# Performance work log

Measured on AMD Instinct MI355X. Metric: run time of the kernel, lower is better.

The kernel has to match this reference:

```python
import jax, jax.numpy as jnp
import numpy as np

B, T, D, H = 4, 2048, 1024, 16
HD = D // H  # 64

def setup_inputs() -> dict:
    key = jax.random.key(0)
    ks = jax.random.split(key, 6)
    s = 0.02
    x = jax.random.normal(ks[0], (B, T, D), dtype=jnp.float32)
    # per-head projection weights, torch Linear layout [out=HD, in=D], stacked over heads
    Wq = jax.random.normal(ks[1], (H, HD, D), dtype=jnp.float32) * s
    Wk = jax.random.normal(ks[2], (H, HD, D), dtype=jnp.float32) * s
    Wv = jax.random.normal(ks[3], (H, HD, D), dtype=jnp.float32) * s
    Wo = jax.random.normal(ks[4], (D, D), dtype=jnp.float32) * s
    bo = jax.random.normal(ks[5], (D,), dtype=jnp.float32) * s
    return {"x": x, "Wq": Wq, "Wk": Wk, "Wv": Wv, "Wo": Wo, "bo": bo}

def reference(x, Wq, Wk, Wv, Wo, bo):
    # per-head projections (same math as per-head nn.Linear, vectorized over heads)
    Q = jnp.einsum('btd,hkd->bhtk', x, Wq)
    K = jnp.einsum('bsd,hkd->bhsk', x, Wk)
    V = jnp.einsum('bsd,hkd->bhsk', x, Wv)
    scale = 1.0 / jnp.sqrt(jnp.asarray(HD, x.dtype))
    logits = jnp.einsum('bhtk,bhsk->bhts', Q, K) * scale  # [B,H,T,S]
    w = jax.nn.softmax(logits, axis=-1)
    out = jnp.einsum('bhts,bhsk->bhtk', w, V)  # [B,H,T,HD]
    # concat heads in order -> [B,T,D]
    cat = jnp.transpose(out, (0, 2, 1, 3)).reshape(B, T, D)
    return cat @ Wo.T + bo
```

## Files before the change

kernel.cpp:

```cpp
#include <hip/hip_runtime.h>
#include <hip/hip_bf16.h>
#include <stdint.h>
#include <math.h>

typedef unsigned short u16;
typedef uint32_t u32;
typedef __bf16 bf16x8 __attribute__((ext_vector_type(8)));
typedef float f32x4 __attribute__((ext_vector_type(4)));
typedef float f32x16 __attribute__((ext_vector_type(16)));
typedef u16 u16x8 __attribute__((ext_vector_type(8)));
typedef u16 u16x4 __attribute__((ext_vector_type(4)));

#define B_ 4
#define T_ 2048
#define D_ 1024
#define H_ 16
#define HD_ 64
#define M_ (B_*T_)

__device__ __forceinline__ u16 f2bf(float f) {
    union { __bf16 h; u16 u; } c;
    c.h = (__bf16)f;
    return c.u;
}

__device__ __forceinline__ void gl16(const u16* g, u16* l) {
    __builtin_amdgcn_global_load_lds(
        (__attribute__((address_space(1))) void*)g,
        (__attribute__((address_space(3))) void*)l, 16, 0, 0);
}

__device__ __forceinline__ f32x4 mfma16(bf16x8 a, bf16x8 b, f32x4 c) {
    return __builtin_amdgcn_mfma_f32_16x16x32_bf16(a, b, c, 0, 0, 0);
}

__device__ __forceinline__ f32x16 mfma32(bf16x8 a, bf16x8 b, f32x16 c) {
    return __builtin_amdgcn_mfma_f32_32x32x16_bf16(a, b, c, 0, 0, 0);
}

__device__ __forceinline__ u32 cvtpk_bf16(float lo, float hi) {
    u32 r;
    asm("v_cvt_pk_bf16_f32 %0, %1, %2" : "=v"(r) : "v"(lo), "v"(hi));
    return r;
}

__device__ __forceinline__ float fexp2(float x) {
    return __builtin_amdgcn_exp2f(x);
}

__global__ __launch_bounds__(256) void precast(
    const float* __restrict__ x,  const float* __restrict__ wq,
    const float* __restrict__ wk, const float* __restrict__ wv,
    const float* __restrict__ wo,
    u16* __restrict__ xb, u16* __restrict__ wqb, u16* __restrict__ wkb,
    u16* __restrict__ wvb, u16* __restrict__ wob)
{
    const int i = (blockIdx.x * 256 + threadIdx.x) * 4;
    const int nx = M_ * D_;
    const float* src; u16* dst; int off;
    if (i < nx) { src = x; dst = xb; off = i; }
    else {
        int j = i - nx;
        int w = j >> 20;
        off = j & ((1 << 20) - 1);
        switch (w) {
            case 0: src = wq; dst = wqb; break;
            case 1: src = wk; dst = wkb; break;
            case 2: src = wv; dst = wvb; break;
            default: src = wo; dst = wob; break;
        }
    }
    float4 v = *(const float4*)&src[off];
    u16x4 p = { f2bf(v.x), f2bf(v.y), f2bf(v.z), f2bf(v.w) };
    *(u16x4*)&dst[off] = p;
}

__device__ __forceinline__ void gemm8_pipe(
    const u16* __restrict__ Xg, const u16* __restrict__ Wg,
    u16* As, u16* Bs,
    const int tid, const int wm, const int wn, const int l15, const int quad,
    f32x4 acc[4][4])
{
    const u16* asrc[4]; int adst[4];
#pragma unroll
    for (int i = 0; i < 4; ++i) {
        int c = tid + i * 512;
        int row = c >> 3, slot = c & 7;
        asrc[i] = Xg + (size_t)row * 1024 + (slot ^ (row & 7)) * 8;
        adst[i] = c * 8;
    }
    const u16* bsrc[2]; int bdst[2];
#pragma unroll
    for (int i = 0; i < 2; ++i) {
        int c = tid + i * 512;
        int row = c >> 3, slot = c & 7;
        bsrc[i] = Wg + (size_t)row * 1024 + (slot ^ (row & 7)) * 8;
        bdst[i] = c * 8;
    }
    const int sw = l15 & 7;
    const int so0 = (quad ^ sw) * 8;
    const int so1 = ((4 + quad) ^ sw) * 8;

#pragma unroll
    for (int tt = 0; tt < 2; ++tt) {
#pragma unroll
        for (int i = 0; i < 4; ++i) gl16(asrc[i] + tt * 64, As + tt * 16384 + adst[i]);
#pragma unroll
        for (int i = 0; i < 2; ++i) gl16(bsrc[i] + tt * 64, Bs + tt * 8192 + bdst[i]);
    }
    asm volatile("s_waitcnt vmcnt(6)" ::: "memory");
    __builtin_amdgcn_s_barrier();

#pragma unroll
    for (int t = 0; t < 16; ++t) {
        const u16* Ab = As + (t % 3) * 16384;
        const u16* Bb = Bs + (t % 3) * 8192;
        if (t + 2 < 16) {
            const int k2 = (t + 2) * 64;
            u16* An = As + ((t + 2) % 3) * 16384;
            u16* Bn = Bs + ((t + 2) % 3) * 8192;
#pragma unroll
            for (int i = 0; i < 4; ++i) gl16(asrc[i] + k2, An + adst[i]);
#pragma unroll
            for (int i = 0; i < 2; ++i) gl16(bsrc[i] + k2, Bn + bdst[i]);
        }
        __builtin_amdgcn_sched_barrier(0);
        bf16x8 af0[4], af1[4], bf0[4], bf1[4];
#pragma unroll
        for (int mf = 0; mf < 4; ++mf) {
            const int rr = (wm * 64 + mf * 16 + l15) * 64;
            af0[mf] = *(const bf16x8*)&Ab[rr + so0];
            af1[mf] = *(const bf16x8*)&Ab[rr + so1];
        }
#pragma unroll
        for (int nf = 0; nf < 4; ++nf) {
            const int rr = (wn * 64 + nf * 16 + l15) * 64;
            bf0[nf] = *(const bf16x8*)&Bb[rr + so0];
            bf1[nf] = *(const bf16x8*)&Bb[rr + so1];
        }
        __builtin_amdgcn_s_setprio(1);
#pragma unroll
        for (int mf = 0; mf < 4; ++mf)
#pragma unroll
            for (int nf = 0; nf < 4; ++nf)
                acc[mf][nf] = mfma16(af0[mf], bf0[nf], acc[mf][nf]);
#pragma unroll
        for (int mf = 0; mf < 4; ++mf)
#pragma unroll
            for (int nf = 0; nf < 4; ++nf)
                acc[mf][nf] = mfma16(af1[mf], bf1[nf], acc[mf][nf]);
        __builtin_amdgcn_s_setprio(0);
        __builtin_amdgcn_sched_barrier(0);
        if (t + 2 < 16)      asm volatile("s_waitcnt vmcnt(6)" ::: "memory");
        else if (t + 1 < 16) asm volatile("s_waitcnt vmcnt(0)" ::: "memory");
        __builtin_amdgcn_s_barrier();
    }
}

__global__ __launch_bounds__(512, 2) void qkv_gemm(
    const u16* __restrict__ Xb, const u16* __restrict__ W3,
    u16* __restrict__ Qo, u16* __restrict__ Ko, u16* __restrict__ Vt)
{
    __shared__ __attribute__((aligned(16))) u16 As[3 * 256 * 64];
    __shared__ __attribute__((aligned(16))) u16 Bs[3 * 128 * 64];

    const int wg = blockIdx.x + 24 * blockIdx.y;
    const int xcd = wg & 7, k = wg >> 3;
    const int by = xcd * 4 + (k / 24);
    const int bx = k % 24;
    const int n0 = bx * 128, m0 = by * 256;
    const u16* Xg = Xb + (size_t)m0 * 1024;
    const u16* Wg = W3 + (size_t)n0 * 1024;
    const int z = n0 >> 10;
    const float qs = (z == 0) ? 0.125f * 1.44269504088896340736f : 1.0f;

    const int tid = threadIdx.x;
    const int lane = tid & 63;
    const int wave = tid >> 6;
    const int wm = wave >> 1, wn = wave & 1;
    const int l15 = lane & 15, quad = lane >> 4;

    f32x4 acc[4][4];
#pragma unroll
    for (int i = 0; i < 4; ++i)
#pragma unroll
        for (int j = 0; j < 4; ++j) acc[i][j] = (f32x4){0.f, 0.f, 0.f, 0.f};

    gemm8_pipe(Xg, Wg, &As[0], &Bs[0], tid, wm, wn, l15, quad, acc);

    if (z == 2) {
#pragma unroll
        for (int mf = 0; mf < 4; ++mf)
#pragma unroll
            for (int nf = 0; nf < 4; ++nf) {
                int row0 = m0 + wm * 64 + mf * 16 + quad * 4;
                int colz = (n0 & 1023) + wn * 64 + nf * 16 + l15;
                int b = row0 >> 11;
                int t = row0 & 2047;
                int h = colz >> 6;
                int hd = colz & 63;
                u16x4 pv = { f2bf(acc[mf][nf][0]), f2bf(acc[mf][nf][1]),
                             f2bf(acc[mf][nf][2]), f2bf(acc[mf][nf][3]) };
                *(u16x4*)&Vt[(((size_t)(b * H_ + h) * HD_ + hd)) * T_ + t] = pv;
            }
    } else {
        u16* Out = (z == 0) ? Qo : Ko;
#pragma unroll
        for (int mf = 0; mf < 4; ++mf)
#pragma unroll
            for (int nf = 0; nf < 4; ++nf)
#pragma unroll
                for (int r = 0; r < 4; ++r) {
                    int row = m0 + wm * 64 + mf * 16 + quad * 4 + r;
                    int colz = (n0 & 1023) + wn * 64 + nf * 16 + l15;
                    int b = row >> 11;
                    int t = row & 2047;
                    int h = colz >> 6;
                    int hd = colz & 63;
                    Out[((b * H_ + h) * T_ + t) * HD_ + hd] = f2bf(acc[mf][nf][r] * qs);
                }
    }
}

__global__ __launch_bounds__(512, 2) void out_gemm(
    const u16* __restrict__ Xb, const u16* __restrict__ W3,
    const float* __restrict__ bias, float* __restrict__ Out)
{
    __shared__ __attribute__((aligned(16))) u16 As[3 * 256 * 64];
    __shared__ __attribute__((aligned(16))) u16 Bs[3 * 128 * 64];

    const int wg = blockIdx.x + 8 * blockIdx.y;
    const int xcd = wg & 7, k = wg >> 3;
    const int by = xcd * 4 + (k / 8);
    const int bx = k & 7;
    const int n0 = bx * 128, m0 = by * 256;
    const u16* Xg = Xb + (size_t)m0 * 1024;
    const u16* Wg = W3 + (size_t)n0 * 1024;

    const int tid = threadIdx.x;
    const int lane = tid & 63;
    const int wave = tid >> 6;
    const int wm = wave >> 1, wn = wave & 1;
    const int l15 = lane & 15, quad = lane >> 4;

    f32x4 acc[4][4];
#pragma unroll
    for (int i = 0; i < 4; ++i)
#pragma unroll
        for (int j = 0; j < 4; ++j) acc[i][j] = (f32x4){0.f, 0.f, 0.f, 0.f};

    gemm8_pipe(Xg, Wg, &As[0], &Bs[0], tid, wm, wn, l15, quad, acc);

#pragma unroll
    for (int mf = 0; mf < 4; ++mf)
#pragma unroll
        for (int nf = 0; nf < 4; ++nf)
#pragma unroll
            for (int r = 0; r < 4; ++r) {
                int row = m0 + wm * 64 + mf * 16 + quad * 4 + r;
                int col = n0 + wn * 64 + nf * 16 + l15;
                Out[(size_t)row * 1024 + col] = acc[mf][nf][r] + bias[col];
            }
}

__global__ __launch_bounds__(512, 2) void attn(
    const u16* __restrict__ Q, const u16* __restrict__ K,
    const u16* __restrict__ Vt_g, u16* __restrict__ O)
{
    __shared__ __attribute__((aligned(16))) u16 Ks[3 * 4096];
    __shared__ __attribute__((aligned(16))) u16 Vts[3 * 4096];
    __shared__ float lps[8 * 64];

    const int tid = threadIdx.x;
    const int lane = tid & 63, w = tid >> 6;
    const int l31 = lane & 31, hi = lane >> 5;

    const int wg = blockIdx.x + (T_ / 512) * (blockIdx.y + H_ * blockIdx.z);
    const int xcd = wg & 7, k8 = wg >> 3;
    const int bh = xcd + 8 * (k8 >> 2);
    const int xq = k8 & 3;
    const int b = bh >> 4, h = bh & 15;
    const int t0 = xq * 512 + w * 64;

    const size_t base = (size_t)bh * T_ * HD_;
    const u16* Kb = K + base;
    const u16* Vtb = Vt_g + base;
    const u16* Qb = Q + base + (size_t)t0 * HD_;

    const int ra = tid >> 3, sa = (tid & 7) ^ (ra & 7);
    const u16* kp = Kb  + (size_t)ra * 64 + sa * 8;
    const u16* vp = Vtb + (size_t)ra * T_ + sa * 8;
    const int ldst = tid * 8;

    int foff[2][4];
#pragma unroll
    for (int nt = 0; nt < 2; ++nt) {
        const int row = nt * 32 + l31;
#pragma unroll
        for (int kb = 0; kb < 4; ++kb)
            foff[nt][kb] = row * 64 + (((kb * 2 + hi) ^ (row & 7)) * 8);
    }

    bf16x8 qf[2][4];
#pragma unroll
    for (int qt = 0; qt < 2; ++qt)
#pragma unroll
        for (int kb = 0; kb < 4; ++kb)
            qf[qt][kb] = *(const bf16x8*)&Qb[(qt * 32 + l31) * 64 + kb * 16 + hi * 8];

    f32x16 zacc;
#pragma unroll
    for (int i = 0; i < 16; ++i) zacc[i] = 0.f;
    f32x16 oacc[2][2];
#pragma unroll
    for (int qt = 0; qt < 2; ++qt)
#pragma unroll
        for (int cb = 0; cb < 2; ++cb) oacc[qt][cb] = zacc;
    float lp[2] = {0.f, 0.f};

#pragma unroll
    for (int tt = 0; tt < 2; ++tt) {
        gl16(kp + (size_t)tt * 64 * 64, &Ks[tt * 4096 + ldst]);
        gl16(vp + (size_t)tt * 64,      &Vts[tt * 4096 + ldst]);
    }
    asm volatile("s_waitcnt vmcnt(2)" ::: "memory");
    __builtin_amdgcn_s_barrier();

    int cur = 0, nx2 = 2;
    for (int t = 0; t < 32; ++t) {
        if (t + 2 < 32) {
            const size_t so = (size_t)(t + 2) * 64;
            gl16(kp + so * 64, &Ks[nx2 * 4096 + ldst]);
            gl16(vp + so,      &Vts[nx2 * 4096 + ldst]);
        }
        __builtin_amdgcn_sched_barrier(0);
        const u16* Kc = &Ks[cur * 4096];
        const u16* Vc = &Vts[cur * 4096];

        bf16x8 pa[2][4];
#pragma unroll
        for (int nt = 0; nt < 2; ++nt) {
            bf16x8 kf[4];
#pragma unroll
            for (int kb = 0; kb < 4; ++kb)
                kf[kb] = *(const bf16x8*)&Kc[foff[nt][kb]];
#pragma unroll
            for (int qt = 0; qt < 2; ++qt) {
                __builtin_amdgcn_s_setprio(1);
                f32x16 sacc = mfma32(kf[0], qf[qt][0], zacc);
                sacc = mfma32(kf[1], qf[qt][1], sacc);
                sacc = mfma32(kf[2], qf[qt][2], sacc);
                sacc = mfma32(kf[3], qf[qt][3], sacc);
                __builtin_amdgcn_s_setprio(0);
                float p[16];
#pragma unroll
                for (int r = 0; r < 16; ++r) p[r] = fexp2(sacc[r]);
                float s01 = (p[0] + p[1]) + (p[2] + p[3]);
                float s23 = (p[4] + p[5]) + (p[6] + p[7]);
                float s45 = (p[8] + p[9]) + (p[10] + p[11]);
                float s67 = (p[12] + p[13]) + (p[14] + p[15]);
                lp[qt] += (s01 + s23) + (s45 + s67);
#pragma unroll
                for (int c = 0; c < 2; ++c) {
                    const int g = c * 8;
                    u32 a0 = cvtpk_bf16(p[g + 0], p[g + 1]);
                    u32 a1 = cvtpk_bf16(p[g + 2], p[g + 3]);
                    u32 b0 = cvtpk_bf16(p[g + 4], p[g + 5]);
                    u32 b1 = cvtpk_bf16(p[g + 6], p[g + 7]);
                    asm("v_permlane32_swap_b32 %0, %1" : "+v"(a0), "+v"(b0));
                    asm("v_permlane32_swap_b32 %0, %1" : "+v"(a1), "+v"(b1));
                    union { u32 wq[4]; bf16x8 v; } uu;
                    uu.wq[0] = a0; uu.wq[1] = a1; uu.wq[2] = b0; uu.wq[3] = b1;
                    pa[qt][nt * 2 + c] = uu.v;
                }
            }
        }
        __builtin_amdgcn_s_setprio(1);
#pragma unroll
        for (int cb = 0; cb < 2; ++cb)
#pragma unroll
            for (int kb = 0; kb < 4; ++kb) {
                bf16x8 vf = *(const bf16x8*)&Vc[foff[cb][kb]];
                oacc[0][cb] = mfma32(pa[0][kb], vf, oacc[0][cb]);
                oacc[1][cb] = mfma32(pa[1][kb], vf, oacc[1][cb]);
            }
        __builtin_amdgcn_s_setprio(0);
        __builtin_amdgcn_sched_barrier(0);
        if (t + 2 < 32)      asm volatile("s_waitcnt vmcnt(2)" ::: "memory");
        else if (t + 1 < 32) asm volatile("s_waitcnt vmcnt(0)" ::: "memory");
        __builtin_amdgcn_s_barrier();
        cur = (cur == 2) ? 0 : cur + 1;
        nx2 = (nx2 == 2) ? 0 : nx2 + 1;
    }

#pragma unroll
    for (int qt = 0; qt < 2; ++qt) {
        lp[qt] += __shfl_xor(lp[qt], 32);
        lps[w * 64 + qt * 32 + l31] = lp[qt];
    }
    asm volatile("s_waitcnt lgkmcnt(0)" ::: "memory");

#pragma unroll
    for (int qt = 0; qt < 2; ++qt)
#pragma unroll
        for (int r = 0; r < 16; ++r) {
            const int trow = (r & 3) + 8 * (r >> 2) + 4 * hi;
            const float dn = 1.f / lps[w * 64 + qt * 32 + trow];
            const int t = t0 + qt * 32 + trow;
#pragma unroll
            for (int cb = 0; cb < 2; ++cb) {
                const int col = h * 64 + cb * 32 + l31;
                O[((size_t)b * T_ + t) * D_ + col] = f2bf(oacc[qt][cb][r] * dn);
            }
        }
}

extern "C" void kernel_launch(void* const* d_in, const int* in_sizes, int n_in,
                              void* d_out, int out_size, void* d_ws, size_t ws_size,
                              hipStream_t stream) {
    const float* x  = (const float*)d_in[0];
    const float* Wq = (const float*)d_in[1];
    const float* Wk = (const float*)d_in[2];
    const float* Wv = (const float*)d_in[3];
    const float* Wo = (const float*)d_in[4];
    const float* bo = (const float*)d_in[5];
    float* out = (float*)d_out;

    const size_t n_qkv = (size_t)B_ * H_ * T_ * HD_;
    const size_t n_w   = (size_t)D_ * D_;
    u16* Qw   = (u16*)d_ws;
    u16* Kw   = Qw + n_qkv;
    u16* Vtw  = Kw + n_qkv;
    u16* XbOw = Vtw + n_qkv;
    u16* Xb   = XbOw;
    u16* Ow   = XbOw;
    u16* Wqb  = XbOw + n_qkv;
    u16* Wkb  = Wqb + n_w;
    u16* Wvb  = Wkb + n_w;
    u16* Wob  = Wvb + n_w;

    dim3 gc(12288);
    precast<<<gc, 256, 0, stream>>>(x, Wq, Wk, Wv, Wo, Xb, Wqb, Wkb, Wvb, Wob);

    dim3 g1(3072 / 128, M_ / 256);
    qkv_gemm<<<g1, 512, 0, stream>>>(Xb, Wqb, Qw, Kw, Vtw);

    dim3 g2(T_ / 512, H_, B_);
    attn<<<g2, 512, 0, stream>>>(Qw, Kw, Vtw, Ow);

    dim3 g3(1024 / 128, M_ / 256);
    out_gemm<<<g3, 512, 0, stream>>>(Ow, Wob, bo, out);
}
```

Measured before the change: 268.3 us.

## Halve GEMM K-tile to 32, raise occupancy to 4 blocks, drop attention setprio

The shared GEMM pipeline now stages K in 32-wide tiles (32 iterations instead of 16) with a new XOR swizzle matched to 4 slots per row. This halves LDS use per block, so both GEMM kernels can request 4 blocks per CU instead of 2, which should help latency hiding. The trade-off is twice as many barriers and waits per block and less MFMA work between them. Separately, the attention kernel no longer raises wave priority around its MFMA sections.

After: 248.4 us. -7.4%, faster.

```diff
diff --git a/kernel.cpp b/kernel.cpp
--- a/kernel.cpp
+++ b/kernel.cpp
@@ -75,94 +75,80 @@
     *(u16x4*)&dst[off] = p;
 }
 
-__device__ __forceinline__ void gemm8_pipe(
+__device__ __forceinline__ void gemm32_pipe(
     const u16* __restrict__ Xg, const u16* __restrict__ Wg,
     u16* As, u16* Bs,
     const int tid, const int wm, const int wn, const int l15, const int quad,
     f32x4 acc[4][4])
 {
-    const u16* asrc[4]; int adst[4];
-#pragma unroll
-    for (int i = 0; i < 4; ++i) {
-        int c = tid + i * 512;
-        int row = c >> 3, slot = c & 7;
-        asrc[i] = Xg + (size_t)row * 1024 + (slot ^ (row & 7)) * 8;
-        adst[i] = c * 8;
-    }
-    const u16* bsrc[2]; int bdst[2];
+    const u16* asrc[2]; int adst[2];
 #pragma unroll
     for (int i = 0; i < 2; ++i) {
         int c = tid + i * 512;
-        int row = c >> 3, slot = c & 7;
-        bsrc[i] = Wg + (size_t)row * 1024 + (slot ^ (row & 7)) * 8;
-        bdst[i] = c * 8;
-    }
-    const int sw = l15 & 7;
-    const int so0 = (quad ^ sw) * 8;
-    const int so1 = ((4 + quad) ^ sw) * 8;
+        int row = c >> 2, slot = c & 3;
+        int xs = slot ^ ((row >> 1) & 3);
+        asrc[i] = Xg + (size_t)row * 1024 + xs * 8;
+        adst[i] = c * 8;
+    }
+    const u16* bsrc; int bdst;
+    {
+        int c = tid;
+        int row = c >> 2, slot = c & 3;
+        int xs = slot ^ ((row >> 1) & 3);
+        bsrc = Wg + (size_t)row * 1024 + xs * 8;
+        bdst = c * 8;
+    }
+    const int so = (quad ^ ((l15 >> 1) & 3)) * 8;
 
 #pragma unroll
     for (int tt = 0; tt < 2; ++tt) {
 #pragma unroll
-        for (int i = 0; i < 4; ++i) gl16(asrc[i] + tt * 64, As + tt * 16384 + adst[i]);
-#pragma unroll
-        for (int i = 0; i < 2; ++i) gl16(bsrc[i] + tt * 64, Bs + tt * 8192 + bdst[i]);
-    }
-    asm volatile("s_waitcnt vmcnt(6)" ::: "memory");
+        for (int i = 0; i < 2; ++i) gl16(asrc[i] + tt * 32, As + tt * 8192 + adst[i]);
+        gl16(bsrc + tt * 32, Bs + tt * 4096 + bdst);
+    }
+    asm volatile("s_waitcnt vmcnt(3)" ::: "memory");
     __builtin_amdgcn_s_barrier();
 
 #pragma unroll
-    for (int t = 0; t < 16; ++t) {
-        const u16* Ab = As + (t % 3) * 16384;
-        const u16* Bb = Bs + (t % 3) * 8192;
-        if (t + 2 < 16) {
-            const int k2 = (t + 2) * 64;
-            u16* An = As + ((t + 2) % 3) * 16384;
-            u16* Bn = Bs + ((t + 2) % 3) * 8192;
-#pragma unroll
-            for (int i = 0; i < 4; ++i) gl16(asrc[i] + k2, An + adst[i]);
-#pragma unroll
-            for (int i = 0; i < 2; ++i) gl16(bsrc[i] + k2, Bn + bdst[i]);
+    for (int t = 0; t < 32; ++t) {
+        const u16* Ab = As + (t % 3) * 8192;
+        const u16* Bb = Bs + (t % 3) * 4096;
+        if (t + 2 < 32) {
+            const int k2 = (t + 2) * 32;
+            u16* An = As + ((t + 2) % 3) * 8192;
+            u16* Bn = Bs + ((t + 2) % 3) * 4096;
+#pragma unroll
+            for (int i = 0; i < 2; ++i) gl16(asrc[i] + k2, An + adst[i]);
+            gl16(bsrc + k2, Bn + bdst);
         }
         __builtin_amdgcn_sched_barrier(0);
-        bf16x8 af0[4], af1[4], bf0[4], bf1[4];
-#pragma unroll
-        for (int mf = 0; mf < 4; ++mf) {
-            const int rr = (wm * 64 + mf * 16 + l15) * 64;
-            af0[mf] = *(const bf16x8*)&Ab[rr + so0];
-            af1[mf] = *(const bf16x8*)&Ab[rr + so1];
-        }
-#pragma unroll
-        for (int nf = 0; nf < 4; ++nf) {
-            const int rr = (wn * 64 + nf * 16 + l15) * 64;
-            bf0[nf] = *(const bf16x8*)&Bb[rr + so0];
-            bf1[nf] = *(const bf16x8*)&Bb[rr + so1];
-        }
+        bf16x8 af[4], bfr[4];
+#pragma unroll
+        for (int mf = 0; mf < 4; ++mf)
+            af[mf] = *(const bf16x8*)&Ab[(wm * 64 + mf * 16 + l15) * 32 + so];
+#pragma unroll
+        for (int nf = 0; nf < 4; ++nf)
+            bfr[nf] = *(const bf16x8*)&Bb[(wn * 64 + nf * 16 + l15) * 32 + so];
         __builtin_amdgcn_s_setprio(1);
 #pragma unroll
         for (int mf = 0; mf < 4; ++mf)
 #pragma unroll
             for (int nf = 0; nf < 4; ++nf)
-                acc[mf][nf] = mfma16(af0[mf], bf0[nf], acc[mf][nf]);
-#pragma unroll
-        for (int mf = 0; mf < 4; ++mf)
-#pragma unroll
-            for (int nf = 0; nf < 4; ++nf)
-                acc[mf][nf] = mfma16(af1[mf], bf1[nf], acc[mf][nf]);
+                acc[mf][nf] = mfma16(af[mf], bfr[nf], acc[mf][nf]);
         __builtin_amdgcn_s_setprio(0);
         __builtin_amdgcn_sched_barrier(0);
-        if (t + 2 < 16)      asm volatile("s_waitcnt vmcnt(6)" ::: "memory");
-        else if (t + 1 < 16) asm volatile("s_waitcnt vmcnt(0)" ::: "memory");
+        if (t + 2 < 32)      asm volatile("s_waitcnt vmcnt(3)" ::: "memory");
+        else if (t + 1 < 32) asm volatile("s_waitcnt vmcnt(0)" ::: "memory");
         __builtin_amdgcn_s_barrier();
     }
 }
 
-__global__ __launch_bounds__(512, 2) void qkv_gemm(
+__global__ __launch_bounds__(512, 4) void qkv_gemm(
     const u16* __restrict__ Xb, const u16* __restrict__ W3,
     u16* __restrict__ Qo, u16* __restrict__ Ko, u16* __restrict__ Vt)
 {
-    __shared__ __attribute__((aligned(16))) u16 As[3 * 256 * 64];
-    __shared__ __attribute__((aligned(16))) u16 Bs[3 * 128 * 64];
+    __shared__ __attribute__((aligned(16))) u16 As[3 * 256 * 32];
+    __shared__ __attribute__((aligned(16))) u16 Bs[3 * 128 * 32];
 
     const int wg = blockIdx.x + 24 * blockIdx.y;
     const int xcd = wg & 7, k = wg >> 3;
@@ -186,7 +172,7 @@
 #pragma unroll
         for (int j = 0; j < 4; ++j) acc[i][j] = (f32x4){0.f, 0.f, 0.f, 0.f};
 
-    gemm8_pipe(Xg, Wg, &As[0], &Bs[0], tid, wm, wn, l15, quad, acc);
+    gemm32_pipe(Xg, Wg, &As[0], &Bs[0], tid, wm, wn, l15, quad, acc);
 
     if (z == 2) {
 #pragma unroll
@@ -222,12 +208,12 @@
     }
 }
 
-__global__ __launch_bounds__(512, 2) void out_gemm(
+__global__ __launch_bounds__(512, 4) void out_gemm(
     const u16* __restrict__ Xb, const u16* __restrict__ W3,
     const float* __restrict__ bias, float* __restrict__ Out)
 {
-    __shared__ __attribute__((aligned(16))) u16 As[3 * 256 * 64];
-    __shared__ __attribute__((aligned(16))) u16 Bs[3 * 128 * 64];
+    __shared__ __attribute__((aligned(16))) u16 As[3 * 256 * 32];
+    __shared__ __attribute__((aligned(16))) u16 Bs[3 * 128 * 32];
 
     const int wg = blockIdx.x + 8 * blockIdx.y;
     const int xcd = wg & 7, k = wg >> 3;
@@ -249,7 +235,7 @@
 #pragma unroll
         for (int j = 0; j < 4; ++j) acc[i][j] = (f32x4){0.f, 0.f, 0.f, 0.f};
 
-    gemm8_pipe(Xg, Wg, &As[0], &Bs[0], tid, wm, wn, l15, quad, acc);
+    gemm32_pipe(Xg, Wg, &As[0], &Bs[0], tid, wm, wn, l15, quad, acc);
 
 #pragma unroll
     for (int mf = 0; mf < 4; ++mf)
@@ -346,12 +332,10 @@
                 kf[kb] = *(const bf16x8*)&Kc[foff[nt][kb]];
 #pragma unroll
             for (int qt = 0; qt < 2; ++qt) {
-                __builtin_amdgcn_s_setprio(1);
                 f32x16 sacc = mfma32(kf[0], qf[qt][0], zacc);
                 sacc = mfma32(kf[1], qf[qt][1], sacc);
                 sacc = mfma32(kf[2], qf[qt][2], sacc);
                 sacc = mfma32(kf[3], qf[qt][3], sacc);
-                __builtin_amdgcn_s_setprio(0);
                 float p[16];
 #pragma unroll
                 for (int r = 0; r < 16; ++r) p[r] = fexp2(sacc[r]);
@@ -375,7 +359,6 @@
                 }
             }
         }
-        __builtin_amdgcn_s_setprio(1);
 #pragma unroll
         for (int cb = 0; cb < 2; ++cb)
 #pragma unroll
@@ -384,7 +367,6 @@
                 oacc[0][cb] = mfma32(pa[0][kb], vf, oacc[0][cb]);
                 oacc[1][cb] = mfma32(pa[1][kb], vf, oacc[1][cb]);
             }
-        __builtin_amdgcn_s_setprio(0);
         __builtin_amdgcn_sched_barrier(0);
         if (t + 2 < 32)      asm volatile("s_waitcnt vmcnt(2)" ::: "memory");
         else if (t + 1 < 32) asm volatile("s_waitcnt vmcnt(0)" ::: "memory");
```
